# Kernel tuning notes

Measured on AMD Instinct MI355X. Metric: run time of the kernel, lower is better.

The kernel has to match this reference:

```python
import jax, jax.numpy as jnp
import numpy as np

N_NODES = 100000
N_EDGES = 800000
DIM = 300
N_GRAPHS = 64
ATOM_VOCAB = 41
WORD_VOCAB = 10000


def setup_inputs() -> dict:
    key = jax.random.key(0)
    ks = jax.random.split(key, 7)
    atoms = jax.random.randint(ks[0], (N_NODES,), 0, ATOM_VOCAB)
    words = jax.random.randint(ks[1], (N_NODES,), 0, WORD_VOCAB)
    x = jnp.stack([atoms, words], axis=-1)  # [N,2] int indices
    edge_index = jax.random.randint(ks[2], (2, N_EDGES), 0, N_NODES)
    batch = jnp.sort(jax.random.randint(ks[3], (N_NODES,), 0, N_GRAPHS))
    atom_table = jax.random.normal(ks[4], (ATOM_VOCAB, DIM), dtype=jnp.float32) * 0.02
    word_table = jax.random.normal(ks[5], (WORD_VOCAB, DIM), dtype=jnp.float32) * 0.02
    W = jax.random.normal(ks[6], (DIM, DIM), dtype=jnp.float32) / np.sqrt(DIM)
    b = jnp.zeros((DIM,), dtype=jnp.float32)
    return {"x": x, "edge_index": edge_index, "batch": batch,
            "atom_table": atom_table, "word_table": word_table,
            "W": W, "b": b, "num_hops": 3}


def reference(x, edge_index, batch, atom_table, word_table, W, b, num_hops):
    n = x.shape[0]
    # GCNConv: add self-loops, symmetric degree normalization
    loops = jnp.arange(n)
    src = jnp.concatenate([edge_index[0], loops])  # [E+N]
    dst = jnp.concatenate([edge_index[1], loops])
    deg = jax.ops.segment_sum(jnp.ones_like(dst, dtype=W.dtype), dst, num_segments=n)
    dinv = jnp.where(deg > 0, jax.lax.rsqrt(deg), 0.0)
    norm = dinv[src] * dinv[dst]  # [E+N]

    # embed_nodes: atom embedding + word embedding
    h = atom_table[x[:, 0]] + word_table[x[:, 1]]  # [N, D]

    # num_hops applications of the SAME GCNConv (shared W, b)
    for _ in range(num_hops):
        hw = h @ W  # [N, D]
        msg = hw[src] * norm[:, None]  # [E+N, D]
        h = jax.ops.segment_sum(msg, dst, num_segments=n) + b

    # global_mean_pool over batch assignment
    sums = jax.ops.segment_sum(h, batch, num_segments=N_GRAPHS)  # [G, D]
    cnt = jax.ops.segment_sum(jnp.ones((n,), h.dtype), batch, num_segments=N_GRAPHS)
    return sums / jnp.maximum(cnt, 1.0)[:, None]
```

## Files before the change

### kernel.cpp

```cpp
#include <hip/hip_runtime.h>
#include <hip/hip_fp16.h>

#define NG 64
#define NGRAPH_C 64

#define RSZ 25000
#define RSZP4 6250
#define NC_MS 128
#define NRNG 4
#define MSB 1024

#define VOC 10000
#define KPAD 10240
#define NKC 160
#define WGK 64

#define NATOM 41
#define NC_A 128
#define ASL 128

__device__ __forceinline__ unsigned f_as_u(float f) { union { float f; unsigned u; } c; c.f = f; return c.u; }
__device__ __forceinline__ float u_as_f(unsigned u) { union { unsigned u; float f; } c; c.u = u; return c.f; }

__device__ __forceinline__ int xcc_id() {
    unsigned x;
    asm volatile("s_getreg_b32 %0, hwreg(HW_REG_XCC_ID)" : "=s"(x));
    return (int)(x & 7u);
}

union H4 { uint2 u2; __half h[4]; };

__global__ __launch_bounds__(MSB) void k_mscount(const int* __restrict__ src, const int* __restrict__ dst,
                                                 unsigned* __restrict__ rep_in,
                                                 unsigned* __restrict__ rep_src,
                                                 int e, int n, int chunk, int nwords) {
    __shared__ unsigned hin[RSZP4];
    __shared__ unsigned hsrc[RSZP4];
    int c = blockIdx.x % NC_MS;
    int r = blockIdx.x / NC_MS;
    int base = r * RSZ;
    int t = threadIdx.x;
    for (int w = t; w < RSZP4; w += MSB) { hin[w] = 0u; hsrc[w] = 0u; }
    __syncthreads();
    int e0 = c * chunk, e1 = min(e, e0 + chunk);
    for (int i = e0 + t; i < e1; i += MSB) {
        int s = src[i], d = dst[i];
        unsigned ud = (unsigned)(d - base);
        unsigned us = (unsigned)(s - base);
        if (ud < (unsigned)RSZ) atomicAdd(&hin[ud >> 2], 1u << ((ud & 3) * 8));
        if (us < (unsigned)RSZ) atomicAdd(&hsrc[us >> 2], 1u << ((us & 3) * 8));
    }
    __syncthreads();
    int lim = min(RSZ, n - base);
    if (lim <= 0) return;
    int plim = (lim + 3) >> 2;
    unsigned* gin  = rep_in  + (size_t)c * nwords + (base >> 2);
    unsigned* gsrc = rep_src + (size_t)c * nwords + (base >> 2);
    for (int w = t; w < plim; w += MSB) { gin[w] = hin[w]; gsrc[w] = hsrc[w]; }
}

__global__ __launch_bounds__(256) void k_msreduce(const unsigned* __restrict__ rep_in,
                                                  unsigned* __restrict__ rep_src,
                                                  float* __restrict__ dinv,
                                                  unsigned* __restrict__ counts_src,
                                                  int n, int nwords) {
    int i4 = blockIdx.x * 256 + threadIdx.x;
    if (i4 >= nwords) return;
    unsigned s0 = 0, s1 = 0, s2 = 0, s3 = 0;
    unsigned r0 = 0, r1 = 0, r2 = 0, r3 = 0;
#pragma unroll 4
    for (int c = 0; c < NC_MS; ++c) {
        unsigned vi = rep_in[(size_t)c * nwords + i4];
        s0 += vi & 0xFFu; s1 += (vi >> 8) & 0xFFu; s2 += (vi >> 16) & 0xFFu; s3 += vi >> 24;
        unsigned vs = rep_src[(size_t)c * nwords + i4];
        rep_src[(size_t)c * nwords + i4] = r0 | (r1 << 8) | (r2 << 16) | (r3 << 24);
        r0 += vs & 0xFFu; r1 += (vs >> 8) & 0xFFu; r2 += (vs >> 16) & 0xFFu; r3 += vs >> 24;
    }
    int i = i4 * 4;
    unsigned sv[4] = {s0, s1, s2, s3};
    unsigned rv[4] = {r0, r1, r2, r3};
#pragma unroll
    for (int q = 0; q < 4; ++q) {
        if (i + q < n) {
            dinv[i + q] = rsqrtf((float)(sv[q] + 1u));
            counts_src[i + q] = rv[q];
        }
    }
}

__global__ __launch_bounds__(256) void k_blocksum(const unsigned* __restrict__ counts,
                                                  unsigned* __restrict__ partials, int n) {
    __shared__ unsigned s[256];
    int base = blockIdx.x * 1024;
    unsigned sum = 0;
    for (int j = threadIdx.x; j < 1024; j += 256) {
        int i = base + j;
        sum += (i < n) ? counts[i] : 0u;
    }
    s[threadIdx.x] = sum;
    __syncthreads();
    for (int off = 128; off > 0; off >>= 1) {
        if (threadIdx.x < (unsigned)off) s[threadIdx.x] += s[threadIdx.x + off];
        __syncthreads();
    }
    if (threadIdx.x == 0) partials[blockIdx.x] = s[0];
}

__global__ __launch_bounds__(128) void k_scanpartials(unsigned* __restrict__ partials, int nb) {
    __shared__ unsigned s[128];
    int t = threadIdx.x;
    s[t] = (t < nb) ? partials[t] : 0u;
    __syncthreads();
    if (t == 0) {
        unsigned run = 0;
        for (int i = 0; i < nb; ++i) { unsigned v = s[i]; s[i] = run; run += v; }
    }
    __syncthreads();
    if (t < nb) partials[t] = s[t];
}

__global__ __launch_bounds__(256) void k_scanblock(const unsigned* __restrict__ counts,
                                                   const unsigned* __restrict__ partials,
                                                   unsigned* __restrict__ row_start, int n) {
    __shared__ unsigned s[256];
    int base = blockIdx.x * 1024;
    int t = threadIdx.x;
    unsigned v[4];
    unsigned tsum = 0;
#pragma unroll
    for (int j = 0; j < 4; ++j) {
        int i = base + t * 4 + j;
        v[j] = (i < n) ? counts[i] : 0u;
        tsum += v[j];
    }
    s[t] = tsum;
    __syncthreads();
    for (int off = 1; off < 256; off <<= 1) {
        unsigned x = (t >= off) ? s[t - off] : 0u;
        __syncthreads();
        s[t] += x;
        __syncthreads();
    }
    unsigned excl = (t > 0 ? s[t - 1] : 0u) + partials[blockIdx.x];
#pragma unroll
    for (int j = 0; j < 4; ++j) {
        int i = base + t * 4 + j;
        if (i < n) {
            row_start[i] = excl;
            excl += v[j];
            if (i == n - 1) row_start[n] = excl;
        }
    }
}

__global__ __launch_bounds__(MSB) void k_msfill(const int* __restrict__ src, const int* __restrict__ dst,
                                                const int* __restrict__ batch,
                                                const unsigned* __restrict__ row_start,
                                                const unsigned* __restrict__ pref,
                                                const float* __restrict__ dinv,
                                                uint2* __restrict__ euv,
                                                int e, int n, int chunk, int nwords) {
    __shared__ unsigned cur[RSZP4];
    int c = blockIdx.x % NC_MS;
    int r = blockIdx.x / NC_MS;
    int base = r * RSZ;
    int t = threadIdx.x;
    for (int w = t; w < RSZP4; w += MSB) cur[w] = 0u;
    __syncthreads();
    int e0 = c * chunk, e1 = min(e, e0 + chunk);
    const unsigned* prefc = pref + (size_t)c * nwords;
    for (int i = e0 + t; i < e1; i += MSB) {
        int s = src[i];
        unsigned us = (unsigned)(s - base);
        if (us < (unsigned)RSZ) {
            int d = dst[i];
            unsigned sh = (us & 3) * 8;
            unsigned old = atomicAdd(&cur[us >> 2], 1u << sh);
            unsigned slot = (old >> sh) & 0xFFu;
            unsigned p8 = (prefc[(unsigned)s >> 2] >> ((s & 3) * 8)) & 0xFFu;
            unsigned pos = row_start[s] + p8 + slot;
            uint2 pv;
            pv.x = (unsigned)d | ((unsigned)batch[d] << 17);
            pv.y = f_as_u(dinv[s] * dinv[d]);
            euv[pos] = pv;
        }
    }
}

__global__ __launch_bounds__(256) void k_wcount(const int* __restrict__ x,
                                                unsigned* __restrict__ wcnt, int n) {
    int j = blockIdx.x * 256 + threadIdx.x;
    if (j >= n) return;
    atomicAdd(&wcnt[x[2 * j + 1]], 1u);
}

__global__ __launch_bounds__(1024) void k_wscan(const unsigned* __restrict__ wcnt,
                                                unsigned* __restrict__ wstart) {
    __shared__ unsigned s[1024];
    int t = threadIdx.x;
    int lo = t * 10;
    unsigned v[10];
    unsigned sum = 0;
    if (lo < VOC) {
#pragma unroll
        for (int q = 0; q < 10; ++q) { v[q] = wcnt[lo + q]; sum += v[q]; }
    }
    s[t] = sum;
    __syncthreads();
    for (int off = 1; off < 1024; off <<= 1) {
        unsigned x = (t >= off) ? s[t - off] : 0u;
        __syncthreads();
        s[t] += x;
        __syncthreads();
    }
    if (lo < VOC) {
        unsigned excl = (t > 0) ? s[t - 1] : 0u;
#pragma unroll
        for (int q = 0; q < 10; ++q) { wstart[lo + q] = excl; excl += v[q]; }
    }
    if (t == 1023) wstart[VOC] = s[1023];
}

__global__ __launch_bounds__(256) void k_wfill(const int* __restrict__ x,
                                               const unsigned* __restrict__ wstart,
                                               unsigned* __restrict__ wcur,
                                               unsigned* __restrict__ sorted, int n) {
    int j = blockIdx.x * 256 + threadIdx.x;
    if (j >= n) return;
    int w = x[2 * j + 1];
    unsigned pos = wstart[w] + atomicAdd(&wcur[w], 1u);
    sorted[pos] = (unsigned)j;
}

__global__ __launch_bounds__(256) void k_twfill(const __half* __restrict__ Y3,
                                                const unsigned* __restrict__ sorted,
                                                const unsigned* __restrict__ wstart,
                                                float* __restrict__ tw) {
    int w = blockIdx.x * 4 + (threadIdx.x >> 6);
    int g = threadIdx.x & 63;
    if (w >= VOC) return;
    unsigned i0 = wstart[w], i1 = wstart[w + 1];
    float s = 0.f;
    unsigned i = i0;
    for (; i + 2 <= i1; i += 2) {
        unsigned j0 = sorted[i], j1 = sorted[i + 1];
        s += __half2float(Y3[(size_t)j0 * NG + g]) + __half2float(Y3[(size_t)j1 * NG + g]);
    }
    if (i < i1) {
        unsigned j0 = sorted[i];
        s += __half2float(Y3[(size_t)j0 * NG + g]);
    }
    tw[(size_t)w * NG + g] = s;
}

__global__ __launch_bounds__(256) void k_amscount(const int* __restrict__ x,
                                                  unsigned* __restrict__ rep_a,
                                                  int n, int chunk) {
    __shared__ unsigned h[NATOM];
    int c = blockIdx.x;
    int t = threadIdx.x;
    if (t < NATOM) h[t] = 0u;
    __syncthreads();
    int j0 = c * chunk, j1 = min(n, j0 + chunk);
    for (int j = j0 + t; j < j1; j += 256) atomicAdd(&h[x[2 * j]], 1u);
    __syncthreads();
    if (t < NATOM) rep_a[c * NATOM + t] = h[t];
}

__global__ __launch_bounds__(64) void k_amsscan(unsigned* __restrict__ rep_a,
                                                unsigned* __restrict__ astart, int n) {
    __shared__ unsigned tot[NATOM];
    int t = threadIdx.x;
    if (t < NATOM) {
        unsigned run = 0;
        for (int c = 0; c < NC_A; ++c) {
            unsigned v = rep_a[c * NATOM + t];
            rep_a[c * NATOM + t] = run;
            run += v;
        }
        tot[t] = run;
    }
    __syncthreads();
    if (t == 0) {
        unsigned run = 0;
        for (int a = 0; a < NATOM; ++a) { astart[a] = run; run += tot[a]; }
        astart[NATOM] = run;
    }
}

__global__ __launch_bounds__(256) void k_amsfill(const int* __restrict__ x,
                                                 const unsigned* __restrict__ astart,
                                                 const unsigned* __restrict__ rep_a,
                                                 unsigned* __restrict__ asorted,
                                                 int n, int chunk) {
    __shared__ unsigned cur[NATOM];
    __shared__ unsigned base[NATOM];
    int c = blockIdx.x;
    int t = threadIdx.x;
    if (t < NATOM) {
        cur[t] = 0u;
        base[t] = astart[t] + rep_a[c * NATOM + t];
    }
    __syncthreads();
    int j0 = c * chunk, j1 = min(n, j0 + chunk);
    for (int j = j0 + t; j < j1; j += 256) {
        int a = x[2 * j];
        unsigned slot = atomicAdd(&cur[a], 1u);
        asorted[base[a] + slot] = (unsigned)j;
    }
}

__global__ __launch_bounds__(256) void k_tafill(const __half* __restrict__ Y3,
                                                const unsigned* __restrict__ asorted,
                                                const unsigned* __restrict__ astart,
                                                float* __restrict__ tap) {
    int wid = blockIdx.x * 4 + (threadIdx.x >> 6);
    if (wid >= NATOM * ASL) return;
    int a  = wid >> 7;
    int sl = wid & (ASL - 1);
    int g  = threadIdx.x & 63;
    unsigned i0 = astart[a], i1 = astart[a + 1];
    unsigned len = i1 - i0;
    unsigned lo = i0 + (unsigned)((unsigned long long)len * sl / ASL);
    unsigned hi = i0 + (unsigned)((unsigned long long)len * (sl + 1) / ASL);
    float s = 0.f;
    unsigned i = lo;
    for (; i + 2 <= hi; i += 2) {
        unsigned j0 = asorted[i], j1 = asorted[i + 1];
        s += __half2float(Y3[(size_t)j0 * NG + g]) + __half2float(Y3[(size_t)j1 * NG + g]);
    }
    if (i < hi) s += __half2float(Y3[(size_t)asorted[i] * NG + g]);
    tap[((size_t)a * ASL + sl) * NG + g] = s;
}

__global__ __launch_bounds__(256) void k_tareduce(const float* __restrict__ tap,
                                                  float* __restrict__ ta) {
    int i = blockIdx.x * 256 + threadIdx.x;
    if (i >= NATOM * NG) return;
    int a = i >> 6;
    int g = i & 63;
    float s = 0.f;
    for (int sl = 0; sl < ASL; ++sl) s += tap[((size_t)a * ASL + sl) * NG + g];
    ta[i] = s;
}

__global__ __launch_bounds__(128) void k_gstart(const int* __restrict__ batch,
                                                int* __restrict__ gstart, int n, int ngraph) {
    int g = threadIdx.x;
    if (g > ngraph) return;
    if (g == ngraph) { gstart[g] = n; return; }
    int lo = 0, hi = n;
    while (lo < hi) {
        int mid = (lo + hi) >> 1;
        if (batch[mid] < g) lo = mid + 1; else hi = mid;
    }
    gstart[g] = lo;
}

__global__ __launch_bounds__(256) void k_y1(const int* __restrict__ batch,
                                            const float* __restrict__ dinv,
                                            const unsigned* __restrict__ row_start,
                                            const uint2* __restrict__ euv,
                                            __half* __restrict__ Y1, int n) {
    int idx = blockIdx.x * 256 + threadIdx.x;
    if (idx >= n * 16) return;
    int j = idx >> 4;
    int c4 = idx & 15;
    int cb = c4 * 4;
    float a0 = 0.f, a1 = 0.f, a2 = 0.f, a3 = 0.f;
    {
        int bj = batch[j];
        float dj = dinv[j];
        float sn = dj * dj;
        a0 += (bj == cb + 0) ? sn : 0.f;
        a1 += (bj == cb + 1) ? sn : 0.f;
        a2 += (bj == cb + 2) ? sn : 0.f;
        a3 += (bj == cb + 3) ? sn : 0.f;
    }
    unsigned e0 = row_start[j], e1 = row_start[j + 1];
    unsigned e = e0;
    for (; e + 4 <= e1; e += 4) {
        uint2 p0 = euv[e], p1 = euv[e + 1], p2 = euv[e + 2], p3 = euv[e + 3];
        int b0 = (int)(p0.x >> 17), b1 = (int)(p1.x >> 17);
        int b2 = (int)(p2.x >> 17), b3 = (int)(p3.x >> 17);
        float v0 = u_as_f(p0.y), v1 = u_as_f(p1.y);
        float v2 = u_as_f(p2.y), v3 = u_as_f(p3.y);
        a0 += ((b0 == cb + 0) ? v0 : 0.f) + ((b1 == cb + 0) ? v1 : 0.f)
            + ((b2 == cb + 0) ? v2 : 0.f) + ((b3 == cb + 0) ? v3 : 0.f);
        a1 += ((b0 == cb + 1) ? v0 : 0.f) + ((b1 == cb + 1) ? v1 : 0.f)
            + ((b2 == cb + 1) ? v2 : 0.f) + ((b3 == cb + 1) ? v3 : 0.f);
        a2 += ((b0 == cb + 2) ? v0 : 0.f) + ((b1 == cb + 2) ? v1 : 0.f)
            + ((b2 == cb + 2) ? v2 : 0.f) + ((b3 == cb + 2) ? v3 : 0.f);
        a3 += ((b0 == cb + 3) ? v0 : 0.f) + ((b1 == cb + 3) ? v1 : 0.f)
            + ((b2 == cb + 3) ? v2 : 0.f) + ((b3 == cb + 3) ? v3 : 0.f);
    }
    for (; e < e1; ++e) {
        uint2 p = euv[e];
        int bd = (int)(p.x >> 17);
        float v = u_as_f(p.y);
        a0 += (bd == cb + 0) ? v : 0.f;
        a1 += (bd == cb + 1) ? v : 0.f;
        a2 += (bd == cb + 2) ? v : 0.f;
        a3 += (bd == cb + 3) ? v : 0.f;
    }
    H4 o;
    o.h[0] = __float2half(a0); o.h[1] = __float2half(a1);
    o.h[2] = __float2half(a2); o.h[3] = __float2half(a3);
    *(uint2*)&Y1[(size_t)j * NG + cb] = o.u2;
}

__global__ __launch_bounds__(256) void k_yprop(const __half* __restrict__ Yin,
                                               const float* __restrict__ dinv,
                                               const unsigned* __restrict__ row_start,
                                               const uint2* __restrict__ euv,
                                               __half* __restrict__ Yout, int n) {
    int idx = blockIdx.x * 256 + threadIdx.x;
    if (idx >= n * 16) return;
    int j = idx >> 4;
    int c4 = idx & 15;
    int cb = c4 * 4;
    float dj = dinv[j];
    float sn = dj * dj;
    H4 s; s.u2 = *(const uint2*)&Yin[(size_t)j * NG + cb];
    float a0 = sn * __half2float(s.h[0]);
    float a1 = sn * __half2float(s.h[1]);
    float a2 = sn * __half2float(s.h[2]);
    float a3 = sn * __half2float(s.h[3]);
    unsigned e0 = row_start[j], e1 = row_start[j + 1];
    unsigned e = e0;
    for (; e + 4 <= e1; e += 4) {
        uint2 p0 = euv[e], p1 = euv[e + 1], p2 = euv[e + 2], p3 = euv[e + 3];
        float v0 = u_as_f(p0.y), v1 = u_as_f(p1.y);
        float v2 = u_as_f(p2.y), v3 = u_as_f(p3.y);
        H4 m0; m0.u2 = *(const uint2*)&Yin[(size_t)(p0.x & 0x1FFFFu) * NG + cb];
        H4 m1; m1.u2 = *(const uint2*)&Yin[(size_t)(p1.x & 0x1FFFFu) * NG + cb];
        H4 m2; m2.u2 = *(const uint2*)&Yin[(size_t)(p2.x & 0x1FFFFu) * NG + cb];
        H4 m3; m3.u2 = *(const uint2*)&Yin[(size_t)(p3.x & 0x1FFFFu) * NG + cb];
        a0 += v0 * __half2float(m0.h[0]) + v1 * __half2float(m1.h[0])
            + v2 * __half2float(m2.h[0]) + v3 * __half2float(m3.h[0]);
        a1 += v0 * __half2float(m0.h[1]) + v1 * __half2float(m1.h[1])
            + v2 * __half2float(m2.h[1]) + v3 * __half2float(m3.h[1]);
        a2 += v0 * __half2float(m0.h[2]) + v1 * __half2float(m1.h[2])
            + v2 * __half2float(m2.h[2]) + v3 * __half2float(m3.h[2]);
        a3 += v0 * __half2float(m0.h[3]) + v1 * __half2float(m1.h[3])
            + v2 * __half2float(m2.h[3]) + v3 * __half2float(m3.h[3]);
    }
    for (; e < e1; ++e) {
        uint2 p0 = euv[e];
        float v0 = u_as_f(p0.y);
        H4 m0; m0.u2 = *(const uint2*)&Yin[(size_t)(p0.x & 0x1FFFFu) * NG + cb];
        a0 += v0 * __half2float(m0.h[0]);
        a1 += v0 * __half2float(m0.h[1]);
        a2 += v0 * __half2float(m0.h[2]);
        a3 += v0 * __half2float(m0.h[3]);
    }
    H4 o;
    o.h[0] = __float2half(a0); o.h[1] = __float2half(a1);
    o.h[2] = __float2half(a2); o.h[3] = __float2half(a3);
    *(uint2*)&Yout[(size_t)j * NG + cb] = o.u2;
}

__global__ __launch_bounds__(256) void k_colsumh(const __half* __restrict__ Y,
                                                 float* __restrict__ su8, int n) {
    __shared__ float red[16][NG];
    int t = threadIdx.x;
    int cg = t & 15;
    int sr = t >> 4;
    float a0 = 0.f, a1 = 0.f, a2 = 0.f, a3 = 0.f;
    int stride = gridDim.x * 16;
    for (int j = blockIdx.x * 16 + sr; j < n; j += stride) {
        H4 v; v.u2 = *(const uint2*)&Y[(size_t)j * NG + cg * 4];
        a0 += __half2float(v.h[0]);
        a1 += __half2float(v.h[1]);
        a2 += __half2float(v.h[2]);
        a3 += __half2float(v.h[3]);
    }
    red[sr][cg * 4 + 0] = a0;
    red[sr][cg * 4 + 1] = a1;
    red[sr][cg * 4 + 2] = a2;
    red[sr][cg * 4 + 3] = a3;
    __syncthreads();
    if (t < NG) {
        float s = 0.f;
#pragma unroll
        for (int q = 0; q < 16; ++q) s += red[q][t];
        int r = xcc_id();
        __hip_atomic_fetch_add(&su8[r * NG + t], s,
                               __ATOMIC_RELAXED, __HIP_MEMORY_SCOPE_WORKGROUP);
    }
}

__global__ __launch_bounds__(256) void k_wgemm2(const float* __restrict__ T,
                                                const float* __restrict__ Tab,
                                                float* __restrict__ Gpart) {
    __shared__ float Asm[32 * 64];
    __shared__ float Bsm[32 * 64];
    const int t = threadIdx.x;
    const int tg = t >> 4;
    const int tc = t & 15;
    const int c0 = blockIdx.x * 64;
    const int kb = blockIdx.y * WGK;

    float acc[4][4] = {};

    for (int sub = 0; sub < WGK / 32; ++sub) {
        int kbase = kb + sub * 32;
#pragma unroll
        for (int r2 = 0; r2 < 2; ++r2) {
            int idx4 = r2 * 256 + t;
            int k = idx4 >> 4, g4 = idx4 & 15;
            float4 v = *(const float4*)&T[(size_t)(kbase + k) * 64 + g4 * 4];
            *(float4*)&Asm[k * 64 + g4 * 4] = v;
        }
#pragma unroll
        for (int r2 = 0; r2 < 2; ++r2) {
            int idx4 = r2 * 256 + t;
            int k = idx4 >> 4, c4i = idx4 & 15;
            int gk = kbase + k;
            int cb2 = c0 + c4i * 4;
            float4 v;
            if (gk < VOC && cb2 + 3 < 300) {
                v = *(const float4*)&Tab[(size_t)gk * 300 + cb2];
            } else {
                float tmp[4];
#pragma unroll
                for (int q = 0; q < 4; ++q)
                    tmp[q] = (gk < VOC && cb2 + q < 300) ? Tab[(size_t)gk * 300 + cb2 + q] : 0.f;
                v.x = tmp[0]; v.y = tmp[1]; v.z = tmp[2]; v.w = tmp[3];
            }
            *(float4*)&Bsm[k * 64 + c4i * 4] = v;
        }
        __syncthreads();
#pragma unroll 8
        for (int k = 0; k < 32; ++k) {
            float4 a4 = *(const float4*)&Asm[k * 64 + tg * 4];
            float4 b4 = *(const float4*)&Bsm[k * 64 + tc * 4];
            float a[4] = {a4.x, a4.y, a4.z, a4.w};
            float b[4] = {b4.x, b4.y, b4.z, b4.w};
#pragma unroll
            for (int i = 0; i < 4; ++i)
#pragma unroll
                for (int jj = 0; jj < 4; ++jj) acc[i][jj] += a[i] * b[jj];
        }
        __syncthreads();
    }

    float* gp = Gpart + (size_t)blockIdx.y * (NG * 300);
#pragma unroll
    for (int i = 0; i < 4; ++i) {
        int g = tg * 4 + i;
#pragma unroll
        for (int jj = 0; jj < 4; ++jj) {
            int c = c0 + tc * 4 + jj;
            if (c < 300) gp[g * 300 + c] = acc[i][jj];
        }
    }
}

__global__ __launch_bounds__(256) void k_greduce(const float* __restrict__ Gpart,
                                                 float* __restrict__ G0) {
    int k = blockIdx.x * 256 + threadIdx.x;
    if (k >= NG * 300) return;
    int p0 = blockIdx.y * (NKC / 8);
    int p1 = p0 + (NKC / 8);
    float s = 0.f;
    for (int p = p0; p < p1; ++p) s += Gpart[(size_t)p * (NG * 300) + k];
    atomicAdd(&G0[k], s);
}

__global__ __launch_bounds__(256) void k_agemm(const float* __restrict__ T,
                                               const float* __restrict__ Tab,
                                               float* __restrict__ G0) {
    int j = blockIdx.x * 256 + threadIdx.x;
    if (j >= NG * 300) return;
    int g = j / 300, c = j - g * 300;
    float acc = 0.f;
#pragma unroll
    for (int k = 0; k < 41; ++k) acc += T[(size_t)k * NG + g] * Tab[(size_t)k * 300 + c];
    atomicAdd(&G0[j], acc);
}

__global__ __launch_bounds__(256) void k_smm(const float* __restrict__ A,
                                             const float* __restrict__ W,
                                             float* __restrict__ C) {
    int j = blockIdx.x * 256 + threadIdx.x;
    if (j >= NG * 300) return;
    int g = j / 300, c = j - g * 300;
    int k0 = blockIdx.y * 60;
    float acc = 0.f;
#pragma unroll 1
    for (int k = k0; k < k0 + 60; k += 4) {
        float a0 = A[g * 300 + k + 0], a1 = A[g * 300 + k + 1];
        float a2 = A[g * 300 + k + 2], a3 = A[g * 300 + k + 3];
        float w0 = W[(k + 0) * 300 + c], w1 = W[(k + 1) * 300 + c];
        float w2 = W[(k + 2) * 300 + c], w3 = W[(k + 3) * 300 + c];
        acc += a0 * w0 + a1 * w1 + a2 * w2 + a3 * w3;
    }
    atomicAdd(&C[j], acc);
}

__global__ __launch_bounds__(256) void k_vec(const float* __restrict__ vin,
                                             const float* __restrict__ W,
                                             float* __restrict__ r_out) {
    int c = blockIdx.x * 256 + threadIdx.x;
    if (c >= 300) return;
    int k0 = blockIdx.y * 75;
    float acc = 0.f;
    for (int k = k0; k < k0 + 75; ++k) acc += vin[k] * W[k * 300 + c];
    atomicAdd(&r_out[c], acc);
}

__global__ __launch_bounds__(256) void k_out(const float* __restrict__ T3,
                                             const float* __restrict__ su1,
                                             const float* __restrict__ su2,
                                             const int* __restrict__ gstart,
                                             const float* __restrict__ r1,
                                             const float* __restrict__ r2,
                                             const float* __restrict__ b,
                                             float* __restrict__ out) {
    int j = blockIdx.x * 256 + threadIdx.x;
    if (j >= NG * 300) return;
    int g = j / 300, c = j - g * 300;
    int cnt = gstart[g + 1] - gstart[g];
    float s1 = 0.f, s2 = 0.f;
#pragma unroll
    for (int r = 0; r < 8; ++r) {
        s1 += su1[r * NG + g];
        s2 += su2[r * NG + g];
    }
    float v = T3[j] + s2 * r2[c] + s1 * r1[c] + (float)cnt * b[c];
    out[j] = v / (float)(cnt > 0 ? cnt : 1);
}

extern "C" void kernel_launch(void* const* d_in, const int* in_sizes, int n_in,
                              void* d_out, int out_size, void* d_ws, size_t ws_size,
                              hipStream_t stream) {
    const int*   x     = (const int*)d_in[0];
    const int*   ei    = (const int*)d_in[1];
    const int*   batch = (const int*)d_in[2];
    const float* at    = (const float*)d_in[3];
    const float* wt    = (const float*)d_in[4];
    const float* W     = (const float*)d_in[5];
    const float* b     = (const float*)d_in[6];

    const int n = in_sizes[0] / 2;
    const int e = in_sizes[1] / 2;

    char* ws = (char*)d_ws;
    size_t off = 0;
    auto carve = [&](size_t bytes) {
        void* p = ws + off;
        off += (bytes + 255) & ~(size_t)255;
        return p;
    };
    __half*   Y1        = (__half*)carve((size_t)n * NG * 2);
    __half*   Y2        = (__half*)carve((size_t)n * NG * 2);
    __half*   Y3        = (__half*)carve((size_t)n * NG * 2);
    uint2*    euv       = (uint2*)carve((size_t)e * 8);
    float*    dinv      = (float*)carve((size_t)n * 4);
    unsigned* counts_src= (unsigned*)carve((size_t)n * 4);
    unsigned* row_start = (unsigned*)carve((size_t)(n + 1) * 4);
    unsigned* partials  = (unsigned*)carve(1024 * 4);
    int*      gstart    = (int*)carve(65 * 4);
    unsigned* wstart    = (unsigned*)carve((size_t)(VOC + 1) * 4);
    unsigned* sorted    = (unsigned*)carve((size_t)n * 4);
    unsigned* asorted   = (unsigned*)carve((size_t)n * 4);
    unsigned* astart    = (unsigned*)carve((NATOM + 1) * 4);
    unsigned* rep_a     = (unsigned*)carve((size_t)NC_A * NATOM * 4);
    float*    tap       = (float*)carve((size_t)NATOM * ASL * NG * 4);
    char*     zB0       = (char*)carve(0);
    float*    su1       = (float*)carve((size_t)8 * NG * 4);
    float*    su2       = (float*)carve((size_t)8 * NG * 4);
    float*    ta        = (float*)carve((size_t)NATOM * NG * 4);
    float*    tw        = (float*)carve((size_t)KPAD * NG * 4);
    float*    G0        = (float*)carve((size_t)NG * 300 * 4);
    float*    r1        = (float*)carve(300 * 4);
    float*    r2        = (float*)carve(300 * 4);
    float*    T1        = (float*)carve((size_t)NG * 300 * 4);
    float*    T2        = (float*)carve((size_t)NG * 300 * 4);
    float*    T3        = (float*)carve((size_t)NG * 300 * 4);
    unsigned* wcnt      = (unsigned*)carve((size_t)VOC * 4);
    unsigned* wcur      = (unsigned*)carve((size_t)VOC * 4);
    char*     zB1       = (char*)carve(0);

    const int* src = ei;
    const int* dst = ei + e;

    unsigned* rep_in  = (unsigned*)Y1;
    unsigned* rep_src = (unsigned*)Y2;
    float*    Gpart   = (float*)Y1;

    hipMemsetAsync(zB0, 0, (size_t)(zB1 - zB0), stream);

    const int nwords = (n + 3) / 4;
    const int chunk  = (e + NC_MS - 1) / NC_MS;
    const int achunk = (n + NC_A - 1) / NC_A;

    k_mscount<<<NRNG * NC_MS, MSB, 0, stream>>>(src, dst, rep_in, rep_src, e, n, chunk, nwords);
    k_msreduce<<<(nwords + 255) / 256, 256, 0, stream>>>(rep_in, rep_src, dinv, counts_src, n, nwords);
    int NB = (n + 1023) / 1024;
    k_blocksum<<<NB, 256, 0, stream>>>(counts_src, partials, n);
    k_scanpartials<<<1, 128, 0, stream>>>(partials, NB);
    k_scanblock<<<NB, 256, 0, stream>>>(counts_src, partials, row_start, n);
    k_msfill<<<NRNG * NC_MS, MSB, 0, stream>>>(src, dst, batch, row_start, rep_src, dinv, euv, e, n, chunk, nwords);
    k_gstart<<<1, 128, 0, stream>>>(batch, gstart, n, NGRAPH_C);

    int nb256 = (n + 255) / 256;
    k_wcount<<<nb256, 256, 0, stream>>>(x, wcnt, n);
    k_wscan<<<1, 1024, 0, stream>>>(wcnt, wstart);
    k_wfill<<<nb256, 256, 0, stream>>>(x, wstart, wcur, sorted, n);

    k_amscount<<<NC_A, 256, 0, stream>>>(x, rep_a, n, achunk);
    k_amsscan<<<1, 64, 0, stream>>>(rep_a, astart, n);
    k_amsfill<<<NC_A, 256, 0, stream>>>(x, astart, rep_a, asorted, n, achunk);

    int yb = (n * 16 + 255) / 256;
    k_y1<<<yb, 256, 0, stream>>>(batch, dinv, row_start, euv, Y1, n);
    k_colsumh<<<512, 256, 0, stream>>>(Y1, su1, n);
    k_yprop<<<yb, 256, 0, stream>>>(Y1, dinv, row_start, euv, Y2, n);
    k_colsumh<<<512, 256, 0, stream>>>(Y2, su2, n);
    k_yprop<<<yb, 256, 0, stream>>>(Y2, dinv, row_start, euv, Y3, n);

    k_tafill<<<(NATOM * ASL + 3) / 4, 256, 0, stream>>>(Y3, asorted, astart, tap);
    k_tareduce<<<(NATOM * NG + 255) / 256, 256, 0, stream>>>(tap, ta);
    k_twfill<<<(VOC + 3) / 4, 256, 0, stream>>>(Y3, sorted, wstart, tw);
    {
        dim3 gw(5, NKC);
        k_wgemm2<<<gw, 256, 0, stream>>>(tw, wt, Gpart);
        dim3 gr((NG * 300 + 255) / 256, 8);
        k_greduce<<<gr, 256, 0, stream>>>(Gpart, G0);
    }
    k_agemm<<<(NG * 300 + 255) / 256, 256, 0, stream>>>(ta, at, G0);

    {
        dim3 gs((NG * 300 + 255) / 256, 5);
        k_smm<<<gs, 256, 0, stream>>>(G0, W, T1);
        k_smm<<<gs, 256, 0, stream>>>(T1, W, T2);
        k_smm<<<gs, 256, 0, stream>>>(T2, W, T3);
        dim3 gv(2, 4);
        k_vec<<<gv, 256, 0, stream>>>(b, W, r1);
        k_vec<<<gv, 256, 0, stream>>>(r1, W, r2);
    }

    k_out<<<(NG * 300 + 255) / 256, 256, 0, stream>>>(T3, su1, su2, gstart, r1, r2, b, (float*)d_out);
}
```

Measured before the change: 325.1 us.

## Merge small preprocessing and tail kernels to cut launch count

Several small kernels are fused into combined launches. Word and atom counting, scanning and filling now share kernels, and the gstart binary search moves into the scan kernel. The tw and ta gathers run in one launch, and the ta reduction, greduce/agemm and vec products ride as extra blocks in the wgemm and smm launches. The word-GEMM K chunking also changes (fewer, larger chunks), which reduces parallelism in exchange for less partial-sum reduction work. The aim is to remove per-launch overhead and serialization between tiny kernels, at the cost of extra branching and some load imbalance inside the fused launches.

```diff
diff --git a/kernel.cpp b/kernel.cpp
--- a/kernel.cpp
+++ b/kernel.cpp
@@ -12,12 +12,14 @@
 
 #define VOC 10000
 #define KPAD 10240
-#define NKC 160
-#define WGK 64
+#define NKC 80
+#define WGK 128
 
 #define NATOM 41
 #define NC_A 128
 #define ASL 128
+#define TW_BLKS ((VOC + 3) / 4)
+#define TA_BLKS ((NATOM * ASL + 3) / 4)
 
 __device__ __forceinline__ unsigned f_as_u(float f) { union { float f; unsigned u; } c; c.f = f; return c.u; }
 __device__ __forceinline__ float u_as_f(unsigned u) { union { unsigned u; float f; } c; c.u = u; return c.f; }
@@ -187,88 +189,32 @@
     }
 }
 
-__global__ __launch_bounds__(256) void k_wcount(const int* __restrict__ x,
-                                                unsigned* __restrict__ wcnt, int n) {
-    int j = blockIdx.x * 256 + threadIdx.x;
-    if (j >= n) return;
-    atomicAdd(&wcnt[x[2 * j + 1]], 1u);
-}
-
-__global__ __launch_bounds__(1024) void k_wscan(const unsigned* __restrict__ wcnt,
-                                                unsigned* __restrict__ wstart) {
-    __shared__ unsigned s[1024];
-    int t = threadIdx.x;
-    int lo = t * 10;
-    unsigned v[10];
-    unsigned sum = 0;
-    if (lo < VOC) {
-#pragma unroll
-        for (int q = 0; q < 10; ++q) { v[q] = wcnt[lo + q]; sum += v[q]; }
-    }
-    s[t] = sum;
-    __syncthreads();
-    for (int off = 1; off < 1024; off <<= 1) {
-        unsigned x = (t >= off) ? s[t - off] : 0u;
-        __syncthreads();
-        s[t] += x;
-        __syncthreads();
-    }
-    if (lo < VOC) {
-        unsigned excl = (t > 0) ? s[t - 1] : 0u;
-#pragma unroll
-        for (int q = 0; q < 10; ++q) { wstart[lo + q] = excl; excl += v[q]; }
-    }
-    if (t == 1023) wstart[VOC] = s[1023];
-}
-
-__global__ __launch_bounds__(256) void k_wfill(const int* __restrict__ x,
-                                               const unsigned* __restrict__ wstart,
-                                               unsigned* __restrict__ wcur,
-                                               unsigned* __restrict__ sorted, int n) {
-    int j = blockIdx.x * 256 + threadIdx.x;
-    if (j >= n) return;
-    int w = x[2 * j + 1];
-    unsigned pos = wstart[w] + atomicAdd(&wcur[w], 1u);
-    sorted[pos] = (unsigned)j;
-}
-
-__global__ __launch_bounds__(256) void k_twfill(const __half* __restrict__ Y3,
-                                                const unsigned* __restrict__ sorted,
-                                                const unsigned* __restrict__ wstart,
-                                                float* __restrict__ tw) {
-    int w = blockIdx.x * 4 + (threadIdx.x >> 6);
-    int g = threadIdx.x & 63;
-    if (w >= VOC) return;
-    unsigned i0 = wstart[w], i1 = wstart[w + 1];
-    float s = 0.f;
-    unsigned i = i0;
-    for (; i + 2 <= i1; i += 2) {
-        unsigned j0 = sorted[i], j1 = sorted[i + 1];
-        s += __half2float(Y3[(size_t)j0 * NG + g]) + __half2float(Y3[(size_t)j1 * NG + g]);
-    }
-    if (i < i1) {
-        unsigned j0 = sorted[i];
-        s += __half2float(Y3[(size_t)j0 * NG + g]);
-    }
-    tw[(size_t)w * NG + g] = s;
-}
-
-__global__ __launch_bounds__(256) void k_amscount(const int* __restrict__ x,
-                                                  unsigned* __restrict__ rep_a,
-                                                  int n, int chunk) {
+__global__ __launch_bounds__(256) void k_xcount(const int* __restrict__ x,
+                                                unsigned* __restrict__ wcnt,
+                                                unsigned* __restrict__ rep_a,
+                                                int n, int chunk) {
     __shared__ unsigned h[NATOM];
     int c = blockIdx.x;
     int t = threadIdx.x;
     if (t < NATOM) h[t] = 0u;
     __syncthreads();
     int j0 = c * chunk, j1 = min(n, j0 + chunk);
-    for (int j = j0 + t; j < j1; j += 256) atomicAdd(&h[x[2 * j]], 1u);
+    for (int j = j0 + t; j < j1; j += 256) {
+        int2 xv = *(const int2*)&x[2 * j];
+        atomicAdd(&h[xv.x], 1u);
+        atomicAdd(&wcnt[xv.y], 1u);
+    }
     __syncthreads();
     if (t < NATOM) rep_a[c * NATOM + t] = h[t];
 }
 
-__global__ __launch_bounds__(64) void k_amsscan(unsigned* __restrict__ rep_a,
-                                                unsigned* __restrict__ astart, int n) {
+__global__ __launch_bounds__(1024) void k_scanall(const unsigned* __restrict__ wcnt,
+                                                  unsigned* __restrict__ wstart,
+                                                  unsigned* __restrict__ rep_a,
+                                                  unsigned* __restrict__ astart,
+                                                  const int* __restrict__ batch,
+                                                  int* __restrict__ gstart, int n) {
+    __shared__ unsigned s[1024];
     __shared__ unsigned tot[NATOM];
     int t = threadIdx.x;
     if (t < NATOM) {
@@ -280,7 +226,38 @@
         }
         tot[t] = run;
     }
-    __syncthreads();
+    if (t <= NGRAPH_C) {
+        if (t == NGRAPH_C) gstart[t] = n;
+        else {
+            int lo = 0, hi = n;
+            while (lo < hi) {
+                int mid = (lo + hi) >> 1;
+                if (batch[mid] < t) lo = mid + 1; else hi = mid;
+            }
+            gstart[t] = lo;
+        }
+    }
+    int lo10 = t * 10;
+    unsigned v[10];
+    unsigned sum = 0;
+    if (lo10 < VOC) {
+#pragma unroll
+        for (int q = 0; q < 10; ++q) { v[q] = wcnt[lo10 + q]; sum += v[q]; }
+    }
+    s[t] = sum;
+    __syncthreads();
+    for (int off = 1; off < 1024; off <<= 1) {
+        unsigned xx = (t >= off) ? s[t - off] : 0u;
+        __syncthreads();
+        s[t] += xx;
+        __syncthreads();
+    }
+    if (lo10 < VOC) {
+        unsigned excl = (t > 0) ? s[t - 1] : 0u;
+#pragma unroll
+        for (int q = 0; q < 10; ++q) { wstart[lo10 + q] = excl; excl += v[q]; }
+    }
+    if (t == 1023) wstart[VOC] = s[1023];
     if (t == 0) {
         unsigned run = 0;
         for (int a = 0; a < NATOM; ++a) { astart[a] = run; run += tot[a]; }
@@ -288,11 +265,14 @@
     }
 }
 
-__global__ __launch_bounds__(256) void k_amsfill(const int* __restrict__ x,
-                                                 const unsigned* __restrict__ astart,
-                                                 const unsigned* __restrict__ rep_a,
-                                                 unsigned* __restrict__ asorted,
-                                                 int n, int chunk) {
+__global__ __launch_bounds__(256) void k_xfill(const int* __restrict__ x,
+                                               const unsigned* __restrict__ wstart,
+                                               unsigned* __restrict__ wcur,
+                                               unsigned* __restrict__ sorted,
+                                               const unsigned* __restrict__ astart,
+                                               const unsigned* __restrict__ rep_a,
+                                               unsigned* __restrict__ asorted,
+                                               int n, int chunk) {
     __shared__ unsigned cur[NATOM];
     __shared__ unsigned base[NATOM];
     int c = blockIdx.x;
@@ -304,57 +284,12 @@
     __syncthreads();
     int j0 = c * chunk, j1 = min(n, j0 + chunk);
     for (int j = j0 + t; j < j1; j += 256) {
-        int a = x[2 * j];
-        unsigned slot = atomicAdd(&cur[a], 1u);
-        asorted[base[a] + slot] = (unsigned)j;
-    }
-}
-
-__global__ __launch_bounds__(256) void k_tafill(const __half* __restrict__ Y3,
-                                                const unsigned* __restrict__ asorted,
-                                                const unsigned* __restrict__ astart,
-                                                float* __restrict__ tap) {
-    int wid = blockIdx.x * 4 + (threadIdx.x >> 6);
-    if (wid >= NATOM * ASL) return;
-    int a  = wid >> 7;
-    int sl = wid & (ASL - 1);
-    int g  = threadIdx.x & 63;
-    unsigned i0 = astart[a], i1 = astart[a + 1];
-    unsigned len = i1 - i0;
-    unsigned lo = i0 + (unsigned)((unsigned long long)len * sl / ASL);
-    unsigned hi = i0 + (unsigned)((unsigned long long)len * (sl + 1) / ASL);
-    float s = 0.f;
-    unsigned i = lo;
-    for (; i + 2 <= hi; i += 2) {
-        unsigned j0 = asorted[i], j1 = asorted[i + 1];
-        s += __half2float(Y3[(size_t)j0 * NG + g]) + __half2float(Y3[(size_t)j1 * NG + g]);
-    }
-    if (i < hi) s += __half2float(Y3[(size_t)asorted[i] * NG + g]);
-    tap[((size_t)a * ASL + sl) * NG + g] = s;
-}
-
-__global__ __launch_bounds__(256) void k_tareduce(const float* __restrict__ tap,
-                                                  float* __restrict__ ta) {
-    int i = blockIdx.x * 256 + threadIdx.x;
-    if (i >= NATOM * NG) return;
-    int a = i >> 6;
-    int g = i & 63;
-    float s = 0.f;
-    for (int sl = 0; sl < ASL; ++sl) s += tap[((size_t)a * ASL + sl) * NG + g];
-    ta[i] = s;
-}
-
-__global__ __launch_bounds__(128) void k_gstart(const int* __restrict__ batch,
-                                                int* __restrict__ gstart, int n, int ngraph) {
-    int g = threadIdx.x;
-    if (g > ngraph) return;
-    if (g == ngraph) { gstart[g] = n; return; }
-    int lo = 0, hi = n;
-    while (lo < hi) {
-        int mid = (lo + hi) >> 1;
-        if (batch[mid] < g) lo = mid + 1; else hi = mid;
-    }
-    gstart[g] = lo;
+        int2 xv = *(const int2*)&x[2 * j];
+        unsigned slot = atomicAdd(&cur[xv.x], 1u);
+        asorted[base[xv.x] + slot] = (unsigned)j;
+        unsigned pos = wstart[xv.y] + atomicAdd(&wcur[xv.y], 1u);
+        sorted[pos] = (unsigned)j;
+    }
 }
 
 __global__ __launch_bounds__(256) void k_y1(const int* __restrict__ batch,
@@ -490,9 +425,62 @@
     }
 }
 
+__global__ __launch_bounds__(256) void k_twta(const __half* __restrict__ Y3,
+                                              const unsigned* __restrict__ sorted,
+                                              const unsigned* __restrict__ wstart,
+                                              float* __restrict__ tw,
+                                              const unsigned* __restrict__ asorted,
+                                              const unsigned* __restrict__ astart,
+                                              float* __restrict__ tap) {
+    int t = threadIdx.x;
+    int g = t & 63;
+    if (blockIdx.x < TW_BLKS) {
+        int w = blockIdx.x * 4 + (t >> 6);
+        if (w >= VOC) return;
+        unsigned i0 = wstart[w], i1 = wstart[w + 1];
+        float s = 0.f;
+        unsigned i = i0;
+        for (; i + 2 <= i1; i += 2) {
+            unsigned j0 = sorted[i], j1 = sorted[i + 1];
+            s += __half2float(Y3[(size_t)j0 * NG + g]) + __half2float(Y3[(size_t)j1 * NG + g]);
+        }
+        if (i < i1) s += __half2float(Y3[(size_t)sorted[i] * NG + g]);
+        tw[(size_t)w * NG + g] = s;
+    } else {
+        int wid = (blockIdx.x - TW_BLKS) * 4 + (t >> 6);
+        if (wid >= NATOM * ASL) return;
+        int a  = wid >> 7;
+        int sl = wid & (ASL - 1);
+        unsigned i0 = astart[a], i1 = astart[a + 1];
+        unsigned len = i1 - i0;
+        unsigned lo = i0 + (unsigned)((unsigned long long)len * sl / ASL);
+        unsigned hi = i0 + (unsigned)((unsigned long long)len * (sl + 1) / ASL);
+        float s = 0.f;
+        unsigned i = lo;
+        for (; i + 2 <= hi; i += 2) {
+            unsigned j0 = asorted[i], j1 = asorted[i + 1];
+            s += __half2float(Y3[(size_t)j0 * NG + g]) + __half2float(Y3[(size_t)j1 * NG + g]);
+        }
+        if (i < hi) s += __half2float(Y3[(size_t)asorted[i] * NG + g]);
+        tap[((size_t)a * ASL + sl) * NG + g] = s;
+    }
+}
+
 __global__ __launch_bounds__(256) void k_wgemm2(const float* __restrict__ T,
                                                 const float* __restrict__ Tab,
-                                                float* __restrict__ Gpart) {
+                                                float* __restrict__ Gpart,
+                                                const float* __restrict__ tap,
+                                                float* __restrict__ ta) {
+    if (blockIdx.x == 5) {
+        int i = blockIdx.y * 256 + threadIdx.x;
+        if (i >= NATOM * NG) return;
+        int a = i >> 6;
+        int g = i & 63;
+        float s = 0.f;
+        for (int sl = 0; sl < ASL; ++sl) s += tap[((size_t)a * ASL + sl) * NG + g];
+        ta[i] = s;
+        return;
+    }
     __shared__ float Asm[32 * 64];
     __shared__ float Bsm[32 * 64];
     const int t = threadIdx.x;
@@ -557,33 +545,43 @@
     }
 }
 
-__global__ __launch_bounds__(256) void k_greduce(const float* __restrict__ Gpart,
-                                                 float* __restrict__ G0) {
+__global__ __launch_bounds__(256) void k_gredagemm(const float* __restrict__ Gpart,
+                                                   const float* __restrict__ ta,
+                                                   const float* __restrict__ at,
+                                                   float* __restrict__ G0) {
     int k = blockIdx.x * 256 + threadIdx.x;
     if (k >= NG * 300) return;
-    int p0 = blockIdx.y * (NKC / 8);
-    int p1 = p0 + (NKC / 8);
-    float s = 0.f;
-    for (int p = p0; p < p1; ++p) s += Gpart[(size_t)p * (NG * 300) + k];
-    atomicAdd(&G0[k], s);
-}
-
-__global__ __launch_bounds__(256) void k_agemm(const float* __restrict__ T,
-                                               const float* __restrict__ Tab,
-                                               float* __restrict__ G0) {
-    int j = blockIdx.x * 256 + threadIdx.x;
-    if (j >= NG * 300) return;
-    int g = j / 300, c = j - g * 300;
-    float acc = 0.f;
-#pragma unroll
-    for (int k = 0; k < 41; ++k) acc += T[(size_t)k * NG + g] * Tab[(size_t)k * 300 + c];
-    atomicAdd(&G0[j], acc);
+    if (blockIdx.y < 8) {
+        int p0 = blockIdx.y * (NKC / 8);
+        int p1 = p0 + (NKC / 8);
+        float s = 0.f;
+        for (int p = p0; p < p1; ++p) s += Gpart[(size_t)p * (NG * 300) + k];
+        atomicAdd(&G0[k], s);
+    } else {
+        int g = k / 300, c = k - g * 300;
+        float acc = 0.f;
+#pragma unroll
+        for (int q = 0; q < NATOM; ++q) acc += ta[q * NG + g] * at[(size_t)q * 300 + c];
+        atomicAdd(&G0[k], acc);
+    }
 }
 
 __global__ __launch_bounds__(256) void k_smm(const float* __restrict__ A,
                                              const float* __restrict__ W,
-                                             float* __restrict__ C) {
-    int j = blockIdx.x * 256 + threadIdx.x;
+                                             float* __restrict__ C,
+                                             const float* __restrict__ vin,
+                                             float* __restrict__ r_out) {
+    int bx = blockIdx.x;
+    if (bx >= 75) {
+        int c = (bx - 75) * 256 + threadIdx.x;
+        if (c >= 300) return;
+        int k0 = blockIdx.y * 60;
+        float acc = 0.f;
+        for (int k = k0; k < k0 + 60; ++k) acc += vin[k] * W[k * 300 + c];
+        atomicAdd(&r_out[c], acc);
+        return;
+    }
+    int j = bx * 256 + threadIdx.x;
     if (j >= NG * 300) return;
     int g = j / 300, c = j - g * 300;
     int k0 = blockIdx.y * 60;
@@ -597,17 +595,6 @@
         acc += a0 * w0 + a1 * w1 + a2 * w2 + a3 * w3;
     }
     atomicAdd(&C[j], acc);
-}
-
-__global__ __launch_bounds__(256) void k_vec(const float* __restrict__ vin,
-                                             const float* __restrict__ W,
-                                             float* __restrict__ r_out) {
-    int c = blockIdx.x * 256 + threadIdx.x;
-    if (c >= 300) return;
-    int k0 = blockIdx.y * 75;
-    float acc = 0.f;
-    for (int k = k0; k < k0 + 75; ++k) acc += vin[k] * W[k * 300 + c];
-    atomicAdd(&r_out[c], acc);
 }
 
 __global__ __launch_bounds__(256) void k_out(const float* __restrict__ T3,
@@ -703,16 +690,10 @@
     k_scanpartials<<<1, 128, 0, stream>>>(partials, NB);
     k_scanblock<<<NB, 256, 0, stream>>>(counts_src, partials, row_start, n);
     k_msfill<<<NRNG * NC_MS, MSB, 0, stream>>>(src, dst, batch, row_start, rep_src, dinv, euv, e, n, chunk, nwords);
-    k_gstart<<<1, 128, 0, stream>>>(batch, gstart, n, NGRAPH_C);
-
-    int nb256 = (n + 255) / 256;
-    k_wcount<<<nb256, 256, 0, stream>>>(x, wcnt, n);
-    k_wscan<<<1, 1024, 0, stream>>>(wcnt, wstart);
-    k_wfill<<<nb256, 256, 0, stream>>>(x, wstart, wcur, sorted, n);
-
-    k_amscount<<<NC_A, 256, 0, stream>>>(x, rep_a, n, achunk);
-    k_amsscan<<<1, 64, 0, stream>>>(rep_a, astart, n);
-    k_amsfill<<<NC_A, 256, 0, stream>>>(x, astart, rep_a, asorted, n, achunk);
+
+    k_xcount<<<NC_A, 256, 0, stream>>>(x, wcnt, rep_a, n, achunk);
+    k_scanall<<<1, 1024, 0, stream>>>(wcnt, wstart, rep_a, astart, batch, gstart, n);
+    k_xfill<<<NC_A, 256, 0, stream>>>(x, wstart, wcur, sorted, astart, rep_a, asorted, n, achunk);
 
     int yb = (n * 16 + 255) / 256;
     k_y1<<<yb, 256, 0, stream>>>(batch, dinv, row_start, euv, Y1, n);
@@ -721,25 +702,20 @@
     k_colsumh<<<512, 256, 0, stream>>>(Y2, su2, n);
     k_yprop<<<yb, 256, 0, stream>>>(Y2, dinv, row_start, euv, Y3, n);
 
-    k_tafill<<<(NATOM * ASL + 3) / 4, 256, 0, stream>>>(Y3, asorted, astart, tap);
-    k_tareduce<<<(NATOM * NG + 255) / 256, 256, 0, stream>>>(tap, ta);
-    k_twfill<<<(VOC + 3) / 4, 256, 0, stream>>>(Y3, sorted, wstart, tw);
+    k_twta<<<TW_BLKS + TA_BLKS, 256, 0, stream>>>(Y3, sorted, wstart, tw, asorted, astart, tap);
     {
-        dim3 gw(5, NKC);
-        k_wgemm2<<<gw, 256, 0, stream>>>(tw, wt, Gpart);
-        dim3 gr((NG * 300 + 255) / 256, 8);
-        k_greduce<<<gr, 256, 0, stream>>>(Gpart, G0);
-    }
-    k_agemm<<<(NG * 300 + 255) / 256, 256, 0, stream>>>(ta, at, G0);
+        dim3 gw(6, NKC);
+        k_wgemm2<<<gw, 256, 0, stream>>>(tw, wt, Gpart, tap, ta);
+        dim3 gr((NG * 300 + 255) / 256, 9);
+        k_gredagemm<<<gr, 256, 0, stream>>>(Gpart, ta, at, G0);
+    }
 
     {
-        dim3 gs((NG * 300 + 255) / 256, 5);
-        k_smm<<<gs, 256, 0, stream>>>(G0, W, T1);
-        k_smm<<<gs, 256, 0, stream>>>(T1, W, T2);
-        k_smm<<<gs, 256, 0, stream>>>(T2, W, T3);
-        dim3 gv(2, 4);
-        k_vec<<<gv, 256, 0, stream>>>(b, W, r1);
-        k_vec<<<gv, 256, 0, stream>>>(r1, W, r2);
+        dim3 gs1(77, 5);
+        k_smm<<<gs1, 256, 0, stream>>>(G0, W, T1, b, r1);
+        k_smm<<<gs1, 256, 0, stream>>>(T1, W, T2, r1, r2);
+        dim3 gs3(75, 5);
+        k_smm<<<gs3, 256, 0, stream>>>(T2, W, T3, r2, r2);
     }
 
     k_out<<<(NG * 300 + 255) / 256, 256, 0, stream>>>(T3, su1, su2, gstart, r1, r2, b, (float*)d_out);
```

Measured after the change: 297.7 us. -8.4%, faster.
